# Kernel tuning notes

Measured on AMD Instinct MI355X. Metric: run time of the kernel, lower is better.

## Reference

```python
import jax, jax.numpy as jnp
import numpy as np

BETA = 0.25
N, D, K = 131072, 128, 1024  # points, embed dim, codebook size


def setup_inputs() -> dict:
    key = jax.random.key(0)
    k1, k2 = jax.random.split(key)
    x = jax.random.normal(k1, (N, D), dtype=jnp.float32)
    emb = jax.random.normal(k2, (K, D), dtype=jnp.float32)  # codebook (nn.Embedding weight)
    return {"x": x, "emb": emb}


def reference(x, emb):
    dist = (jnp.sum(x * x, axis=1, keepdims=True)
            + jnp.sum(emb * emb, axis=1)
            - 2.0 * (x @ emb.T))
    index = jnp.argmin(dist, axis=1)          # [N]
    # one_hot @ emb == gather of nearest code
    quantized = emb[index]                    # [N, D]
    commitment_loss = jnp.mean((jax.lax.stop_gradient(quantized) - x) ** 2)
    embedding_loss = jnp.mean((quantized - jax.lax.stop_gradient(x)) ** 2)
    vq_loss = commitment_loss * BETA + embedding_loss
    # straight-through estimator
    quantized_st = x + jax.lax.stop_gradient(quantized - x)
    return index[:, None], quantized_st, vq_loss
```

## Files before the change

kernel.cpp:

```cpp
#include <hip/hip_runtime.h>

#define NPTS 131072
#define DIM  128
#define KC   1024
#define CHB  16640

using half8 = __attribute__((ext_vector_type(8))) _Float16;
using f32x4 = __attribute__((ext_vector_type(4))) float;

static __device__ __forceinline__ unsigned umax_(unsigned a, unsigned b){ return a > b ? a : b; }
static __device__ __forceinline__ unsigned med3u(unsigned a, unsigned b, unsigned c){
    unsigned d;
    asm("v_med3_u32 %0, %1, %2, %3" : "=v"(d) : "v"(a), "v"(b), "v"(c));
    return d;
}


__global__ void vq_prep(const float* __restrict__ emb, unsigned short* __restrict__ wsE,
                        float* __restrict__ eeW) {
    int lane = threadIdx.x & 63, wv = threadIdx.x >> 6;
    int code = blockIdx.x * 4 + wv;
    const float* e = emb + (size_t)code * DIM;
    float a = e[lane], b = e[lane + 64];

    int chunk = code >> 6, r = code & 63, swz = (r & 7) << 4;
    size_t base = (size_t)chunk * 16384 + (size_t)(r << 8);
    _Float16 ha = (_Float16)a, hb = (_Float16)b;
    wsE[(base + (size_t)(((lane << 1))        ^ swz)) >> 1] = __builtin_bit_cast(unsigned short, ha);
    wsE[(base + (size_t)(((lane + 64) << 1)   ^ swz)) >> 1] = __builtin_bit_cast(unsigned short, hb);

    float v = a * a + b * b;
    #pragma unroll
    for (int o = 32; o > 0; o >>= 1) v += __shfl_down(v, o);
    if (lane == 0) eeW[code] = 0.5f * v - 512.0f;
}

__global__
__attribute__((amdgpu_flat_work_group_size(256, 256)))
__attribute__((amdgpu_waves_per_eu(4, 4)))
void vq_mfma(const float* __restrict__ x,
             const float* __restrict__ emb,
             const unsigned short* __restrict__ wsE,
             const float* __restrict__ eeW,
             float* __restrict__ out,
             float* __restrict__ bsum) {
    __shared__ __attribute__((aligned(128))) char lds[2][CHB];
    const int tid  = threadIdx.x;
    const int lane = tid & 63, wv = tid >> 6;
    const int g    = lane >> 4, c = lane & 15;
    const int blockbase = blockIdx.x * 128;

    half8 ah[2][4];
    #pragma unroll
    for (int rt = 0; rt < 2; ++rt) {
        const float* xr = x + (size_t)(blockbase + wv * 32 + rt * 16 + c) * DIM;
        #pragma unroll
        for (int kc = 0; kc < 4; ++kc) {
            const float4* p = reinterpret_cast<const float4*>(xr + kc * 32 + g * 8);
            float4 v0 = p[0], v1 = p[1];
            half8 hh;
            hh[0] = (_Float16)v0.x; hh[1] = (_Float16)v0.y;
            hh[2] = (_Float16)v0.z; hh[3] = (_Float16)v0.w;
            hh[4] = (_Float16)v1.x; hh[5] = (_Float16)v1.y;
            hh[6] = (_Float16)v1.z; hh[7] = (_Float16)v1.w;
            ah[rt][kc] = hh;
        }
    }

    unsigned m1[8], m2[8], m3[8];
    #pragma unroll
    for (int i = 0; i < 8; ++i) { m1[i] = 0u; m2[i] = 0u; m3[i] = 0u; }

    #define STAGE(BUF, CH)                                                                   \
        do {                                                                                 \
            const char* src_ = (const char*)wsE + (size_t)(CH) * 16384 + (size_t)wv * 4096;  \
            char* dst_ = &lds[(BUF)][0] + wv * 4096;                                         \
            _Pragma("unroll")                                                                \
            for (int it = 0; it < 4; ++it) {                                                 \
                __builtin_amdgcn_global_load_lds(                                            \
                    (const __attribute__((address_space(1))) void*)(src_ + it * 1024 + lane * 16), \
                    (__attribute__((address_space(3))) void*)(dst_ + it * 1024),             \
                    16, 0, 0);                                                               \
            }                                                                                \
            if (wv == 0) {                                                                   \
                __builtin_amdgcn_global_load_lds(                                            \
                    (const __attribute__((address_space(1))) void*)(eeW + (size_t)(CH) * 64 + lane), \
                    (__attribute__((address_space(3))) void*)(&lds[(BUF)][0] + 16384),       \
                    4, 0, 0);                                                                \
            }                                                                                \
        } while (0)

    #define PRELOAD(L_, CT_)                                                                 \
        do {                                                                                 \
            const int rp_  = (CT_) * 16 + c;                                                 \
            const int swp_ = (rp_ & 7) << 4;                                                 \
            _Pragma("unroll")                                                                \
            for (int kc = 0; kc < 4; ++kc)                                                   \
                bq[kc] = *reinterpret_cast<const half8*>((L_) + (rp_ << 8) + (((kc << 6) + (g << 4)) ^ swp_)); \
            eecq = *reinterpret_cast<const float*>((L_) + 16384 + (rp_ << 2));               \
        } while (0)

    half8 bq[4]; float eecq;

    STAGE(0, 0);
    __syncthreads();
    PRELOAD(&lds[0][0], 0);

    for (int ch = 0; ch < 16; ++ch) {
        if (ch < 15) STAGE((ch + 1) & 1, ch + 1);
        const char* L = &lds[ch & 1][0];

        #pragma unroll
        for (int ct = 0; ct < 4; ++ct) {
            half8 b0 = bq[0], b1v = bq[1], b2v = bq[2], b3v = bq[3];
            const float eec = eecq;
            if (ct < 3) PRELOAD(L, ct + 1);

            f32x4 acc0 = {-eec, -eec, -eec, -eec};
            f32x4 acc1 = {-eec, -eec, -eec, -eec};
            acc0 = __builtin_amdgcn_mfma_f32_16x16x32_f16(ah[0][0], b0,  acc0, 0, 0, 0);
            acc1 = __builtin_amdgcn_mfma_f32_16x16x32_f16(ah[1][0], b0,  acc1, 0, 0, 0);
            acc0 = __builtin_amdgcn_mfma_f32_16x16x32_f16(ah[0][1], b1v, acc0, 0, 0, 0);
            acc1 = __builtin_amdgcn_mfma_f32_16x16x32_f16(ah[1][1], b1v, acc1, 0, 0, 0);
            acc0 = __builtin_amdgcn_mfma_f32_16x16x32_f16(ah[0][2], b2v, acc0, 0, 0, 0);
            acc1 = __builtin_amdgcn_mfma_f32_16x16x32_f16(ah[1][2], b2v, acc1, 0, 0, 0);
            acc0 = __builtin_amdgcn_mfma_f32_16x16x32_f16(ah[0][3], b3v, acc0, 0, 0, 0);
            acc1 = __builtin_amdgcn_mfma_f32_16x16x32_f16(ah[1][3], b3v, acc1, 0, 0, 0);

            const unsigned codeC = (unsigned)(1023 - (ch * 64 + ct * 16 + c));
            #pragma unroll
            for (int q = 0; q < 4; ++q) {
                #pragma unroll
                for (int rt = 0; rt < 2; ++rt) {
                    float sp = (rt ? acc1[q] : acc0[q]);
                    unsigned u   = __builtin_bit_cast(unsigned, sp);
                    unsigned key = (u & 0xFFFFFC00u) | codeC;
                    const int i = rt * 4 + q;
                    m3[i] = med3u(m2[i], m3[i], key);
                    m2[i] = med3u(m1[i], m2[i], key);
                    m1[i] = umax_(m1[i], key);
                }
            }
        }
        __syncthreads();
        if (ch < 15) PRELOAD(&lds[(ch + 1) & 1][0], 0);
    }

    int* lbest = reinterpret_cast<int*>(&lds[0][0]);
    #pragma unroll
    for (int rt = 0; rt < 2; ++rt) {
        #pragma unroll
        for (int q = 0; q < 4; ++q) {
            const int i = rt * 4 + q;
            unsigned a1 = m1[i], a2 = m2[i], a3 = m3[i];
            #pragma unroll
            for (int mk = 1; mk < 16; mk <<= 1) {
                unsigned b1 = (unsigned)__shfl_xor((int)a1, mk, 64);
                unsigned b2 = (unsigned)__shfl_xor((int)a2, mk, 64);
                unsigned b3 = (unsigned)__shfl_xor((int)a3, mk, 64);
                unsigned c1 = umax_(a1, b1), t1 = (a1 < b1 ? a1 : b1);
                unsigned u1 = umax_(a2, b2), u2 = (a2 < b2 ? a2 : b2);
                unsigned c2 = umax_(t1, u1), t2 = (t1 < u1 ? t1 : u1);
                unsigned c3 = umax_(umax_(t2, u2), umax_(a3, b3));
                a1 = c1; a2 = c2; a3 = c3;
            }
            if (c == 0) {
                int lr = wv * 32 + rt * 16 + g * 4 + q;
                int i1 = 1023 - (int)(a1 & 1023u);
                int i2 = 1023 - (int)(a2 & 1023u);
                int i3 = 1023 - (int)(a3 & 1023u);
                lbest[lr] = i1 | (i2 << 10) | (i3 << 20);
            }
        }
    }
    __syncthreads();

    {
        const int lrow = tid >> 1, hf = tid & 1;
        const int grow = blockbase + lrow;
        const int pk = lbest[lrow];
        const int ia = pk & 1023, ib = (pk >> 10) & 1023, ic = (pk >> 20) & 1023;

        const float4* xv4 = reinterpret_cast<const float4*>(x + (size_t)grow * DIM + hf * 64);
        const float4* ea = reinterpret_cast<const float4*>(emb + (size_t)ia * DIM + hf * 64);
        const float4* eb = reinterpret_cast<const float4*>(emb + (size_t)ib * DIM + hf * 64);
        const float4* ec = reinterpret_cast<const float4*>(emb + (size_t)ic * DIM + hf * 64);
        float da = 0.f, db = 0.f, dc = 0.f;
        #pragma unroll 4
        for (int i = 0; i < 16; ++i) {
            float4 xx = xv4[i];
            float4 va = ea[i], vb = eb[i], vc = ec[i];
            float ax = va.x - xx.x, ay = va.y - xx.y, az = va.z - xx.z, aw = va.w - xx.w;
            float bx = vb.x - xx.x, by = vb.y - xx.y, bz = vb.z - xx.z, bw = vb.w - xx.w;
            float cx = vc.x - xx.x, cy = vc.y - xx.y, cz = vc.z - xx.z, cw = vc.w - xx.w;
            da += ax * ax + ay * ay + az * az + aw * aw;
            db += bx * bx + by * by + bz * bz + bw * bw;
            dc += cx * cx + cy * cy + cz * cz + cw * cw;
        }
        da += __shfl_xor(da, 1, 64);
        db += __shfl_xor(db, 1, 64);
        dc += __shfl_xor(dc, 1, 64);

        int idx = ia; float dm = da;
        if (db < dm || (db == dm && ib < idx)) { dm = db; idx = ib; }
        if (dc < dm || (dc == dm && ic < idx)) { dm = dc; idx = ic; }

        if (hf == 0) out[grow] = (float)idx;

        const float4* q4 = reinterpret_cast<const float4*>(emb + (size_t)idx * DIM + hf * 64);
        float4* oq = reinterpret_cast<float4*>(out + (size_t)NPTS + (size_t)grow * DIM + hf * 64);
        #pragma unroll
        for (int i = 0; i < 16; ++i) oq[i] = q4[i];

        float lsum = (hf == 0) ? dm : 0.f;
        __shared__ float red[4];
        #pragma unroll
        for (int o = 32; o > 0; o >>= 1) lsum += __shfl_down(lsum, o);
        if (lane == 0) red[wv] = lsum;
        __syncthreads();
        if (tid == 0) bsum[blockIdx.x] = (red[0] + red[1]) + (red[2] + red[3]);
    }
    #undef STAGE
    #undef PRELOAD
}

__global__ void vq_finalize(const float* __restrict__ bsum, float* __restrict__ out) {
    __shared__ float red[16];
    int t = threadIdx.x;
    float v = bsum[t];
    #pragma unroll
    for (int o = 32; o > 0; o >>= 1) v += __shfl_down(v, o);
    if ((t & 63) == 0) red[t >> 6] = v;
    __syncthreads();
    if (t == 0) {
        float s = 0.f;
        #pragma unroll
        for (int i = 0; i < 16; ++i) s += red[i];
        out[(size_t)NPTS + (size_t)NPTS * DIM] = 1.25f * s / 16777216.0f;
    }
}

__global__ void vq_ee(const float* __restrict__ emb, float* __restrict__ eeW) {
    int gid  = blockIdx.x * blockDim.x + threadIdx.x;
    int w    = gid >> 6;
    int lane = threadIdx.x & 63;
    const float* e = emb + (size_t)w * DIM;
    float a = e[lane];
    float b = e[lane + 64];
    float v = a * a + b * b;
    #pragma unroll
    for (int o = 32; o > 0; o >>= 1) v += __shfl_down(v, o);
    if (lane == 0) eeW[w] = 0.5f * v - 512.0f;
}

__global__ __launch_bounds__(256, 1) void vq_main(const float* __restrict__ x,
                                                  const float* __restrict__ emb,
                                                  const float* __restrict__ eeW,
                                                  float* __restrict__ out,
                                                  float* __restrict__ bsum) {
    const int p = blockIdx.x * 256 + threadIdx.x;
    float4 xr[32];
    const float4* xv = reinterpret_cast<const float4*>(x + (size_t)p * DIM);
    #pragma unroll
    for (int i = 0; i < 32; ++i) xr[i] = xv[i];
    float bestv = -3.4e38f; int bi = 0;
    for (int k = 0; k < KC; ++k) {
        const int ku = __builtin_amdgcn_readfirstlane(k);
        const float4* e4 = reinterpret_cast<const float4*>(emb + (size_t)ku * DIM);
        float a0 = 0.f, a1 = 0.f, a2 = 0.f, a3 = 0.f;
        #pragma unroll
        for (int i = 0; i < 32; ++i) {
            float4 ev = e4[i];
            a0 = fmaf(xr[i].x, ev.x, a0);
            a1 = fmaf(xr[i].y, ev.y, a1);
            a2 = fmaf(xr[i].z, ev.z, a2);
            a3 = fmaf(xr[i].w, ev.w, a3);
        }
        float s = ((a0 + a1) + (a2 + a3)) - eeW[ku];
        if (s > bestv) { bestv = s; bi = k; }
    }
    out[p] = (float)bi;
    const float4* q4 = reinterpret_cast<const float4*>(emb + (size_t)bi * DIM);
    float4* oq = reinterpret_cast<float4*>(out + (size_t)NPTS + (size_t)p * DIM);
    float lsum = 0.f;
    #pragma unroll
    for (int i = 0; i < 32; ++i) {
        float4 qv = q4[i];
        oq[i] = qv;
        float dx = qv.x - xr[i].x;
        float dy = qv.y - xr[i].y;
        float dz = qv.z - xr[i].z;
        float dw = qv.w - xr[i].w;
        lsum += dx * dx + dy * dy + dz * dz + dw * dw;
    }
    __shared__ float red[4];
    #pragma unroll
    for (int o = 32; o > 0; o >>= 1) lsum += __shfl_down(lsum, o);
    int lane = threadIdx.x & 63, wvl = threadIdx.x >> 6;
    if (lane == 0) red[wvl] = lsum;
    __syncthreads();
    if (threadIdx.x == 0) bsum[blockIdx.x] = (red[0] + red[1]) + (red[2] + red[3]);
}

__global__ void vq_finalize512(const float* __restrict__ bsum, float* __restrict__ out) {
    __shared__ float red[8];
    int t = threadIdx.x;
    float v = bsum[t];
    #pragma unroll
    for (int o = 32; o > 0; o >>= 1) v += __shfl_down(v, o);
    if ((t & 63) == 0) red[t >> 6] = v;
    __syncthreads();
    if (t == 0) {
        float s = 0.f;
        #pragma unroll
        for (int i = 0; i < 8; ++i) s += red[i];
        out[(size_t)NPTS + (size_t)NPTS * DIM] = 1.25f * s / 16777216.0f;
    }
}

extern "C" void kernel_launch(void* const* d_in, const int* in_sizes, int n_in,
                              void* d_out, int out_size, void* d_ws, size_t ws_size,
                              hipStream_t stream) {
    const float* x   = (const float*)d_in[0];
    const float* emb = (const float*)d_in[1];
    float* out = (float*)d_out;
    char*  ws  = (char*)d_ws;

    if (ws_size >= 270336) {
        unsigned short* wsE = (unsigned short*)ws;
        float* eeW  = (float*)(ws + 262144);
        float* bsum = (float*)(ws + 266240);
        vq_prep<<<256, 256, 0, stream>>>(emb, wsE, eeW);
        vq_mfma<<<1024, 256, 0, stream>>>(x, emb, wsE, eeW, out, bsum);
        vq_finalize<<<1, 1024, 0, stream>>>(bsum, out);
    } else {
        float* eeW  = (float*)ws;
        float* bsum = (float*)ws + 1024;
        vq_ee<<<256, 256, 0, stream>>>(emb, eeW);
        vq_main<<<512, 256, 0, stream>>>(x, emb, eeW, out, bsum);
        vq_finalize512<<<1, 512, 0, stream>>>(bsum, out);
    }
}
```

Baseline: 115.8 us.

## Store codebook in MFMA fragment order and drop register prefetch of B operands

The prep kernel now writes the fp16 codebook in the exact per-lane fragment order the MFMA consumes, so each lane reads a contiguous 16 bytes at lane*16 with no XOR swizzle arithmetic. The software-pipelined register prefetch of the next code tile is removed, and B fragments and norms are loaded from LDS directly inside the loop. The launch bounds change from a fixed four waves per EU to `__launch_bounds__(256,1)`, which frees the register budget. The risk is exposed LDS latency now that the prefetch is gone, and possibly lower occupancy if register use grows.

```diff
diff --git a/kernel.cpp b/kernel.cpp
--- a/kernel.cpp
+++ b/kernel.cpp
@@ -23,11 +23,13 @@
     const float* e = emb + (size_t)code * DIM;
     float a = e[lane], b = e[lane + 64];
 
-    int chunk = code >> 6, r = code & 63, swz = (r & 7) << 4;
-    size_t base = (size_t)chunk * 16384 + (size_t)(r << 8);
+    int chunk = code >> 6, r = code & 63;
+    int ct = r >> 4, c = r & 15;
+    int kc = lane >> 5, g = (lane >> 3) & 3, j = lane & 7;
+    size_t off = (size_t)chunk * 16384 + (size_t)(ct * 4096 + kc * 1024 + g * 256 + c * 16 + j * 2);
     _Float16 ha = (_Float16)a, hb = (_Float16)b;
-    wsE[(base + (size_t)(((lane << 1))        ^ swz)) >> 1] = __builtin_bit_cast(unsigned short, ha);
-    wsE[(base + (size_t)(((lane + 64) << 1)   ^ swz)) >> 1] = __builtin_bit_cast(unsigned short, hb);
+    wsE[off >> 1]          = __builtin_bit_cast(unsigned short, ha);
+    wsE[(off + 2048) >> 1] = __builtin_bit_cast(unsigned short, hb);
 
     float v = a * a + b * b;
     #pragma unroll
@@ -35,15 +37,12 @@
     if (lane == 0) eeW[code] = 0.5f * v - 512.0f;
 }
 
-__global__
-__attribute__((amdgpu_flat_work_group_size(256, 256)))
-__attribute__((amdgpu_waves_per_eu(4, 4)))
-void vq_mfma(const float* __restrict__ x,
-             const float* __restrict__ emb,
-             const unsigned short* __restrict__ wsE,
-             const float* __restrict__ eeW,
-             float* __restrict__ out,
-             float* __restrict__ bsum) {
+__global__ __launch_bounds__(256, 1) void vq_mfma(const float* __restrict__ x,
+                                                  const float* __restrict__ emb,
+                                                  const unsigned short* __restrict__ wsE,
+                                                  const float* __restrict__ eeW,
+                                                  float* __restrict__ out,
+                                                  float* __restrict__ bsum) {
     __shared__ __attribute__((aligned(128))) char lds[2][CHB];
     const int tid  = threadIdx.x;
     const int lane = tid & 63, wv = tid >> 6;
@@ -90,42 +89,31 @@
             }                                                                                \
         } while (0)
 
-    #define PRELOAD(L_, CT_)                                                                 \
-        do {                                                                                 \
-            const int rp_  = (CT_) * 16 + c;                                                 \
-            const int swp_ = (rp_ & 7) << 4;                                                 \
-            _Pragma("unroll")                                                                \
-            for (int kc = 0; kc < 4; ++kc)                                                   \
-                bq[kc] = *reinterpret_cast<const half8*>((L_) + (rp_ << 8) + (((kc << 6) + (g << 4)) ^ swp_)); \
-            eecq = *reinterpret_cast<const float*>((L_) + 16384 + (rp_ << 2));               \
-        } while (0)
-
-    half8 bq[4]; float eecq;
-
     STAGE(0, 0);
     __syncthreads();
-    PRELOAD(&lds[0][0], 0);
 
     for (int ch = 0; ch < 16; ++ch) {
         if (ch < 15) STAGE((ch + 1) & 1, ch + 1);
-        const char* L = &lds[ch & 1][0];
+        const char* L  = &lds[ch & 1][0];
+        const char* Lf = L + (size_t)(lane << 4);
 
         #pragma unroll
         for (int ct = 0; ct < 4; ++ct) {
-            half8 b0 = bq[0], b1v = bq[1], b2v = bq[2], b3v = bq[3];
-            const float eec = eecq;
-            if (ct < 3) PRELOAD(L, ct + 1);
-
+            const float eec = *reinterpret_cast<const float*>(L + 16384 + ((ct * 16 + c) << 2));
             f32x4 acc0 = {-eec, -eec, -eec, -eec};
             f32x4 acc1 = {-eec, -eec, -eec, -eec};
-            acc0 = __builtin_amdgcn_mfma_f32_16x16x32_f16(ah[0][0], b0,  acc0, 0, 0, 0);
-            acc1 = __builtin_amdgcn_mfma_f32_16x16x32_f16(ah[1][0], b0,  acc1, 0, 0, 0);
-            acc0 = __builtin_amdgcn_mfma_f32_16x16x32_f16(ah[0][1], b1v, acc0, 0, 0, 0);
-            acc1 = __builtin_amdgcn_mfma_f32_16x16x32_f16(ah[1][1], b1v, acc1, 0, 0, 0);
-            acc0 = __builtin_amdgcn_mfma_f32_16x16x32_f16(ah[0][2], b2v, acc0, 0, 0, 0);
-            acc1 = __builtin_amdgcn_mfma_f32_16x16x32_f16(ah[1][2], b2v, acc1, 0, 0, 0);
-            acc0 = __builtin_amdgcn_mfma_f32_16x16x32_f16(ah[0][3], b3v, acc0, 0, 0, 0);
-            acc1 = __builtin_amdgcn_mfma_f32_16x16x32_f16(ah[1][3], b3v, acc1, 0, 0, 0);
+            half8 b0 = *reinterpret_cast<const half8*>(Lf + (ct * 4096 + 0 * 1024));
+            half8 b1 = *reinterpret_cast<const half8*>(Lf + (ct * 4096 + 1 * 1024));
+            half8 b2 = *reinterpret_cast<const half8*>(Lf + (ct * 4096 + 2 * 1024));
+            half8 b3 = *reinterpret_cast<const half8*>(Lf + (ct * 4096 + 3 * 1024));
+            acc0 = __builtin_amdgcn_mfma_f32_16x16x32_f16(ah[0][0], b0, acc0, 0, 0, 0);
+            acc1 = __builtin_amdgcn_mfma_f32_16x16x32_f16(ah[1][0], b0, acc1, 0, 0, 0);
+            acc0 = __builtin_amdgcn_mfma_f32_16x16x32_f16(ah[0][1], b1, acc0, 0, 0, 0);
+            acc1 = __builtin_amdgcn_mfma_f32_16x16x32_f16(ah[1][1], b1, acc1, 0, 0, 0);
+            acc0 = __builtin_amdgcn_mfma_f32_16x16x32_f16(ah[0][2], b2, acc0, 0, 0, 0);
+            acc1 = __builtin_amdgcn_mfma_f32_16x16x32_f16(ah[1][2], b2, acc1, 0, 0, 0);
+            acc0 = __builtin_amdgcn_mfma_f32_16x16x32_f16(ah[0][3], b3, acc0, 0, 0, 0);
+            acc1 = __builtin_amdgcn_mfma_f32_16x16x32_f16(ah[1][3], b3, acc1, 0, 0, 0);
 
             const unsigned codeC = (unsigned)(1023 - (ch * 64 + ct * 16 + c));
             #pragma unroll
@@ -143,7 +131,6 @@
             }
         }
         __syncthreads();
-        if (ch < 15) PRELOAD(&lds[(ch + 1) & 1][0], 0);
     }
 
     int* lbest = reinterpret_cast<int*>(&lds[0][0]);
@@ -221,7 +208,6 @@
         if (tid == 0) bsum[blockIdx.x] = (red[0] + red[1]) + (red[2] + red[3]);
     }
     #undef STAGE
-    #undef PRELOAD
 }
 
 __global__ void vq_finalize(const float* __restrict__ bsum, float* __restrict__ out) {
```

Measured after the change: 124.2 us. 7.3% more time.
